# Kernel optimization log

Measured on AMD Instinct MI355X. Metric: run time of the kernel, lower is better.

## Reference

```python
import jax, jax.numpy as jnp
import numpy as np

N, F, HID, C = 8192, 256, 128, 64
ALPHA = 0.2  # LeakyReLU negative slope
NEG = -9e15  # mask value from the torch code


def xavier(key, shape, gain=1.414):
    fan_in, fan_out = shape[0], shape[1]
    limit = gain * np.sqrt(6.0 / (fan_in + fan_out))
    return jax.random.uniform(key, shape, jnp.float32, -limit, limit)


def setup_inputs() -> dict:
    key = jax.random.key(0)
    ks = jax.random.split(key, 6)
    features = jax.random.normal(ks[0], (N, F), jnp.float32)
    support = (jax.random.uniform(ks[1], (N, N)) > 0.995).astype(jnp.float32)
    support = support.at[jnp.arange(N), jnp.arange(N)].set(1.0)
    W0 = xavier(ks[2], (2 * F, HID))
    a0 = xavier(ks[3], (2 * HID, 1))
    W1 = xavier(ks[4], (2 * HID, C))
    a1 = xavier(ks[5], (2 * C, 1))
    return {"features": features, "support": support, "W0": W0, "a0": a0, "W1": W1, "a1": a1}


def gat_layer(x, adj, W, a, concat):
    # precalc=False branch: support = spmm(adj, x); cat with x
    s = adj @ x                               # (N, Fin)
    sup = jnp.concatenate([s, x], axis=1)     # (N, 2*Fin)
    h = sup @ W                               # (N, Fout)
    Fout = h.shape[1]
    # cat([h_i, h_j]) @ a == h_i @ a[:Fout] + h_j @ a[Fout:]  (same math, no N*N*2F tensor)
    src = h @ a[:Fout, 0]                     # (N,)
    dst = h @ a[Fout:, 0]                     # (N,)
    e = jax.nn.leaky_relu(src[:, None] + dst[None, :], ALPHA)  # (N, N)
    e = jnp.where(adj > 0, e, NEG)            # adjacency-masked scores
    att = jax.nn.softmax(e, axis=1)           # (N, N); dropout is identity in eval
    hp = att @ h                              # (N, Fout)
    return jax.nn.elu(hp) if concat else hp


def reference(features, support, W0, a0, W1, a1):
    x = gat_layer(features, support, W0, a0, concat=True)
    out = gat_layer(x, support, W1, a1, concat=False)
    return jax.nn.log_softmax(out, axis=1)
```

## Files before the change

### kernel.cpp

```cpp
#include <hip/hip_runtime.h>
#include <math.h>
#include <stdint.h>

#define NROWS 8192
#define EDGE_CAP 128

using f4v = __attribute__((ext_vector_type(4))) float;

__device__ __forceinline__ uint16_t bfpack(float f) {
    uint32_t x = __float_as_uint(f);
    return (uint16_t)((x + 0x7FFFu + ((x >> 16) & 1u)) >> 16);
}
__device__ __forceinline__ float bfun(uint16_t u) {
    return __uint_as_float((uint32_t)u << 16);
}

__global__ __launch_bounds__(256) void fused_csr_gemm1(const float* __restrict__ adj,
                                                       int* __restrict__ cnt,
                                                       int* __restrict__ col,
                                                       const float* __restrict__ A,
                                                       const float* __restrict__ W,
                                                       float* __restrict__ Y,
                                                       float* __restrict__ Z) {
    __shared__ float As[16][64];
    __shared__ float Bs[16][128];
    int gb  = blockIdx.x;
    int tid = threadIdx.x;

    if (gb < 256) {
        int bm = gb & 127, bn = gb >> 7;
        int tx = tid & 15, ty = tid >> 4;
        const float* Wb = W + (size_t)bn * 256 * 128;
        float acc[4][8] = {};
        for (int k0 = 0; k0 < 256; k0 += 16) {
            {
                int r = tid >> 2, kk = (tid & 3) * 4;
                float4 v = *(const float4*)&A[(size_t)(bm * 64 + r) * 256 + k0 + kk];
                As[kk + 0][r] = v.x; As[kk + 1][r] = v.y;
                As[kk + 2][r] = v.z; As[kk + 3][r] = v.w;
            }
            {
                int kk = tid >> 4, c = (tid & 15) * 8;
                *(float4*)&Bs[kk][c]     = *(const float4*)&Wb[(size_t)(k0 + kk) * 128 + c];
                *(float4*)&Bs[kk][c + 4] = *(const float4*)&Wb[(size_t)(k0 + kk) * 128 + c + 4];
            }
            __syncthreads();
            #pragma unroll
            for (int kk = 0; kk < 16; ++kk) {
                float a[4], b[8];
                #pragma unroll
                for (int i = 0; i < 4; ++i) a[i] = As[kk][ty * 4 + i];
                #pragma unroll
                for (int j = 0; j < 8; ++j) b[j] = Bs[kk][tx * 8 + j];
                #pragma unroll
                for (int i = 0; i < 4; ++i)
                    #pragma unroll
                    for (int j = 0; j < 8; ++j) acc[i][j] += a[i] * b[j];
            }
            __syncthreads();
        }
        float* O = bn ? Z : Y;
        #pragma unroll
        for (int i = 0; i < 4; ++i) {
            int r = bm * 64 + ty * 4 + i;
            float4 v0 = {acc[i][0], acc[i][1], acc[i][2], acc[i][3]};
            float4 v1 = {acc[i][4], acc[i][5], acc[i][6], acc[i][7]};
            *(float4*)&O[(size_t)r * 128 + tx * 8]     = v0;
            *(float4*)&O[(size_t)r * 128 + tx * 8 + 4] = v1;
        }
    } else {
        int row  = (gb - 256) * 4 + (tid >> 6);
        int lane = tid & 63;
        const f4v* arow = (const f4v*)(adj + (size_t)row * NROWS);
        int* crow = col + (size_t)row * EDGE_CAP;
        int count = 0;
        for (int it = 0; it < NROWS / 256; ++it) {
            f4v v = __builtin_nontemporal_load(&arow[it * 64 + lane]);
            float vv[4] = {v.x, v.y, v.z, v.w};
            #pragma unroll
            for (int p = 0; p < 4; ++p) {
                bool nz = vv[p] > 0.0f;
                unsigned long long m = __ballot(nz);
                if (nz) {
                    int off = count + __popcll(m & ((1ull << lane) - 1ull));
                    if (off < EDGE_CAP) crow[off] = it * 256 + lane * 4 + p;
                }
                count += __popcll(m);
            }
        }
        if (lane == 0) cnt[row] = count < EDGE_CAP ? count : EDGE_CAP;
    }
}

__global__ __launch_bounds__(256) void spmm_scores_128(const int* __restrict__ cnt,
                                                       const int* __restrict__ col,
                                                       const float* __restrict__ Y,
                                                       const float* __restrict__ Z,
                                                       const float* __restrict__ a,
                                                       float* __restrict__ H,
                                                       float* __restrict__ src,
                                                       float* __restrict__ dst) {
    __shared__ int sbuf[4][EDGE_CAP];
    int wav  = threadIdx.x >> 6;
    int lane = threadIdx.x & 63;
    int row  = blockIdx.x * 4 + wav;
    int n    = cnt[row];
    const int* cr = col + (size_t)row * EDGE_CAP;
    for (int e = lane; e < n; e += 64) sbuf[wav][e] = cr[e];

    const float2* Y2 = (const float2*)Y;
    float2 s = {0.0f, 0.0f};
    int e = 0;
    for (; e + 8 <= n; e += 8) {
        float2 v[8];
        #pragma unroll
        for (int u = 0; u < 8; ++u) {
            int j = sbuf[wav][e + u];
            v[u] = Y2[(size_t)j * 64 + lane];
        }
        #pragma unroll
        for (int u = 0; u < 8; ++u) { s.x += v[u].x; s.y += v[u].y; }
    }
    for (; e < n; ++e) {
        int j = sbuf[wav][e];
        float2 v = Y2[(size_t)j * 64 + lane];
        s.x += v.x; s.y += v.y;
    }
    float2 z = ((const float2*)Z)[(size_t)row * 64 + lane];
    float hx = s.x + z.x, hy = s.y + z.y;
    float2 hv = {hx, hy};
    ((float2*)H)[(size_t)row * 64 + lane] = hv;
    float s1 = hx * a[lane * 2] + hy * a[lane * 2 + 1];
    float s2 = hx * a[128 + lane * 2] + hy * a[128 + lane * 2 + 1];
    #pragma unroll
    for (int off = 32; off; off >>= 1) {
        s1 += __shfl_xor(s1, off);
        s2 += __shfl_xor(s2, off);
    }
    if (lane == 0) { src[row] = s1; dst[row] = s2; }
}

__global__ __launch_bounds__(256) void attn_agg_gemm2(const int* __restrict__ cnt,
                                                      const int* __restrict__ col,
                                                      const float* __restrict__ H,
                                                      const float* __restrict__ src,
                                                      const float* __restrict__ dst,
                                                      const float* __restrict__ W1,
                                                      float* __restrict__ Y2,
                                                      float* __restrict__ Z2) {
    __shared__ float pbuf[4][EDGE_CAP];
    __shared__ int   cbuf[4][EDGE_CAP];
    __shared__ float xrow[4][128];
    int wav  = threadIdx.x >> 6;
    int lane = threadIdx.x & 63;
    int row  = blockIdx.x * 4 + wav;
    int n    = cnt[row];
    const int* cr = col + (size_t)row * EDGE_CAP;
    float si = src[row];

    float m = -3.0e38f;
    for (int e = lane; e < n; e += 64) {
        int j = cr[e];
        float x = si + dst[j];
        x = x > 0.0f ? x : 0.2f * x;
        cbuf[wav][e] = j;
        pbuf[wav][e] = x;
        m = fmaxf(m, x);
    }
    #pragma unroll
    for (int off = 32; off; off >>= 1) m = fmaxf(m, __shfl_xor(m, off));

    float ssum = 0.0f;
    for (int e = lane; e < n; e += 64) {
        float p = __expf(pbuf[wav][e] - m);
        pbuf[wav][e] = p;
        ssum += p;
    }
    #pragma unroll
    for (int off = 32; off; off >>= 1) ssum += __shfl_xor(ssum, off);
    float inv = 1.0f / ssum;

    const float2* H2 = (const float2*)H;
    float2 o = {0.0f, 0.0f};
    int e = 0;
    for (; e + 8 <= n; e += 8) {
        float2 v[8]; float p[8];
        #pragma unroll
        for (int u = 0; u < 8; ++u) {
            int j = cbuf[wav][e + u];
            p[u] = pbuf[wav][e + u];
            v[u] = H2[(size_t)j * 64 + lane];
        }
        #pragma unroll
        for (int u = 0; u < 8; ++u) { o.x += p[u] * v[u].x; o.y += p[u] * v[u].y; }
    }
    for (; e < n; ++e) {
        int j = cbuf[wav][e];
        float p = pbuf[wav][e];
        float2 v = H2[(size_t)j * 64 + lane];
        o.x += p * v.x; o.y += p * v.y;
    }
    float vx = o.x * inv, vy = o.y * inv;
    vx = vx > 0.0f ? vx : (__expf(vx) - 1.0f);
    vy = vy > 0.0f ? vy : (__expf(vy) - 1.0f);

    float2 hv = {vx, vy};
    ((float2*)&xrow[wav][0])[lane] = hv;

    float y = 0.0f, z = 0.0f;
    #pragma unroll 8
    for (int k = 0; k < 128; ++k) {
        float xk = xrow[wav][k];
        y += xk * W1[(size_t)k * 64 + lane];
        z += xk * W1[(size_t)(128 + k) * 64 + lane];
    }
    Y2[(size_t)row * 64 + lane] = y;
    Z2[(size_t)row * 64 + lane] = z;
}

__global__ __launch_bounds__(256) void spmm_scores_64(const int* __restrict__ cnt,
                                                      const int* __restrict__ col,
                                                      const float* __restrict__ Y,
                                                      const float* __restrict__ Z,
                                                      const float* __restrict__ a,
                                                      uint16_t* __restrict__ Hb,
                                                      float* __restrict__ src,
                                                      float* __restrict__ dst) {
    __shared__ int sbuf[4][EDGE_CAP];
    int wav  = threadIdx.x >> 6;
    int lane = threadIdx.x & 63;
    int row  = blockIdx.x * 4 + wav;
    int n    = cnt[row];
    const int* cr = col + (size_t)row * EDGE_CAP;
    for (int e = lane; e < n; e += 64) sbuf[wav][e] = cr[e];

    float s = 0.0f;
    int e = 0;
    for (; e + 8 <= n; e += 8) {
        float v[8];
        #pragma unroll
        for (int u = 0; u < 8; ++u) v[u] = Y[(size_t)sbuf[wav][e + u] * 64 + lane];
        #pragma unroll
        for (int u = 0; u < 8; ++u) s += v[u];
    }
    for (; e < n; ++e) s += Y[(size_t)sbuf[wav][e] * 64 + lane];
    float h = s + Z[(size_t)row * 64 + lane];
    Hb[(size_t)row * 64 + lane] = bfpack(h);
    float s1 = h * a[lane];
    float s2 = h * a[64 + lane];
    #pragma unroll
    for (int off = 32; off; off >>= 1) {
        s1 += __shfl_xor(s1, off);
        s2 += __shfl_xor(s2, off);
    }
    if (lane == 0) { src[row] = s1; dst[row] = s2; }
}

__global__ __launch_bounds__(256) void attn_agg_final(const int* __restrict__ cnt,
                                                      const int* __restrict__ col,
                                                      const uint16_t* __restrict__ Hb,
                                                      const float* __restrict__ src,
                                                      const float* __restrict__ dst,
                                                      float* __restrict__ out) {
    __shared__ float pbuf[4][EDGE_CAP];
    __shared__ int   cbuf[4][EDGE_CAP];
    int wav  = threadIdx.x >> 6;
    int lane = threadIdx.x & 63;
    int row  = blockIdx.x * 4 + wav;
    int n    = cnt[row];
    const int* cr = col + (size_t)row * EDGE_CAP;
    float si = src[row];

    float m = -3.0e38f;
    for (int e = lane; e < n; e += 64) {
        int j = cr[e];
        float x = si + dst[j];
        x = x > 0.0f ? x : 0.2f * x;
        cbuf[wav][e] = j;
        pbuf[wav][e] = x;
        m = fmaxf(m, x);
    }
    #pragma unroll
    for (int off = 32; off; off >>= 1) m = fmaxf(m, __shfl_xor(m, off));

    float ssum = 0.0f;
    for (int e = lane; e < n; e += 64) {
        float p = __expf(pbuf[wav][e] - m);
        pbuf[wav][e] = p;
        ssum += p;
    }
    #pragma unroll
    for (int off = 32; off; off >>= 1) ssum += __shfl_xor(ssum, off);
    float inv = 1.0f / ssum;

    float o = 0.0f;
    int e = 0;
    for (; e + 8 <= n; e += 8) {
        uint16_t v[8]; float p[8];
        #pragma unroll
        for (int u = 0; u < 8; ++u) {
            p[u] = pbuf[wav][e + u];
            v[u] = Hb[(size_t)cbuf[wav][e + u] * 64 + lane];
        }
        #pragma unroll
        for (int u = 0; u < 8; ++u) o += p[u] * bfun(v[u]);
    }
    for (; e < n; ++e) o += pbuf[wav][e] * bfun(Hb[(size_t)cbuf[wav][e] * 64 + lane]);

    float logit = o * inv;
    float mm = logit;
    #pragma unroll
    for (int off = 32; off; off >>= 1) mm = fmaxf(mm, __shfl_xor(mm, off));
    float se = __expf(logit - mm);
    #pragma unroll
    for (int off = 32; off; off >>= 1) se += __shfl_xor(se, off);
    out[(size_t)row * 64 + lane] = logit - mm - logf(se);
}

extern "C" void kernel_launch(void* const* d_in, const int* in_sizes, int n_in,
                              void* d_out, int out_size, void* d_ws, size_t ws_size,
                              hipStream_t stream) {
    const float* feat = (const float*)d_in[0];
    const float* adj  = (const float*)d_in[1];
    const float* W0   = (const float*)d_in[2];
    const float* a0   = (const float*)d_in[3];
    const float* W1   = (const float*)d_in[4];
    const float* a1   = (const float*)d_in[5];
    float* out = (float*)d_out;

    char* w = (char*)d_ws;
    int* cnt      = (int*)w;        w += (size_t)NROWS * sizeof(int);
    int* col      = (int*)w;        w += (size_t)NROWS * EDGE_CAP * sizeof(int);
    float* Y1   = (float*)w;        w += (size_t)NROWS * 128 * sizeof(float);
    float* Z1   = (float*)w;        w += (size_t)NROWS * 128 * sizeof(float);
    float* H1   = (float*)w;        w += (size_t)NROWS * 128 * sizeof(float);
    float* Y2   = (float*)w;        w += (size_t)NROWS * 64 * sizeof(float);
    float* Z2   = (float*)w;        w += (size_t)NROWS * 64 * sizeof(float);
    uint16_t* H2b = (uint16_t*)w;   w += (size_t)NROWS * 64 * sizeof(uint16_t);
    float* src1 = (float*)w;        w += (size_t)NROWS * sizeof(float);
    float* dst1 = (float*)w;        w += (size_t)NROWS * sizeof(float);
    float* src2 = (float*)w;        w += (size_t)NROWS * sizeof(float);
    float* dst2 = (float*)w;        w += (size_t)NROWS * sizeof(float);

    fused_csr_gemm1<<<256 + NROWS / 4, 256, 0, stream>>>(adj, cnt, col, feat, W0, Y1, Z1);

    spmm_scores_128<<<NROWS / 4, 256, 0, stream>>>(cnt, col, Y1, Z1, a0, H1, src1, dst1);
    attn_agg_gemm2<<<NROWS / 4, 256, 0, stream>>>(cnt, col, H1, src1, dst1, W1, Y2, Z2);

    spmm_scores_64<<<NROWS / 4, 256, 0, stream>>>(cnt, col, Y2, Z2, a1, H2b, src2, dst2);
    attn_agg_final<<<NROWS / 4, 256, 0, stream>>>(cnt, col, H2b, src2, dst2, out);
}
```

Before: 430.6 us.

## Merge four sparse stage kernels into one persistent kernel with grid barriers

Replaces the four per-stage launches (spmm+scores, attention+gemm2, spmm+scores, final attention) with a single persistent kernel of 1024 blocks, each processing two rows per wave, separated by atomic-counter grid barriers. The barrier counter is reset by the first kernel. The goal is to remove kernel launch gaps and tail effects between the small stages. It relies on all 1024 blocks being co-resident, or the barrier spin will deadlock, and it adds barrier spin and serialization overhead.

```diff
diff --git a/kernel.cpp b/kernel.cpp
--- a/kernel.cpp
+++ b/kernel.cpp
@@ -4,6 +4,7 @@
 
 #define NROWS 8192
 #define EDGE_CAP 128
+#define PGRID 1024
 
 using f4v = __attribute__((ext_vector_type(4))) float;
 
@@ -21,11 +22,13 @@
                                                        const float* __restrict__ A,
                                                        const float* __restrict__ W,
                                                        float* __restrict__ Y,
-                                                       float* __restrict__ Z) {
+                                                       float* __restrict__ Z,
+                                                       int* __restrict__ bar) {
     __shared__ float As[16][64];
     __shared__ float Bs[16][128];
     int gb  = blockIdx.x;
     int tid = threadIdx.x;
+    if (gb == 0 && tid == 0) *bar = 0;
 
     if (gb < 256) {
         int bm = gb & 127, bn = gb >> 7;
@@ -92,229 +95,212 @@
     }
 }
 
-__global__ __launch_bounds__(256) void spmm_scores_128(const int* __restrict__ cnt,
-                                                       const int* __restrict__ col,
-                                                       const float* __restrict__ Y,
-                                                       const float* __restrict__ Z,
-                                                       const float* __restrict__ a,
-                                                       float* __restrict__ H,
-                                                       float* __restrict__ src,
-                                                       float* __restrict__ dst) {
-    __shared__ int sbuf[4][EDGE_CAP];
-    int wav  = threadIdx.x >> 6;
-    int lane = threadIdx.x & 63;
-    int row  = blockIdx.x * 4 + wav;
-    int n    = cnt[row];
-    const int* cr = col + (size_t)row * EDGE_CAP;
-    for (int e = lane; e < n; e += 64) sbuf[wav][e] = cr[e];
-
-    const float2* Y2 = (const float2*)Y;
-    float2 s = {0.0f, 0.0f};
-    int e = 0;
-    for (; e + 8 <= n; e += 8) {
-        float2 v[8];
-        #pragma unroll
-        for (int u = 0; u < 8; ++u) {
-            int j = sbuf[wav][e + u];
-            v[u] = Y2[(size_t)j * 64 + lane];
-        }
-        #pragma unroll
-        for (int u = 0; u < 8; ++u) { s.x += v[u].x; s.y += v[u].y; }
-    }
-    for (; e < n; ++e) {
-        int j = sbuf[wav][e];
-        float2 v = Y2[(size_t)j * 64 + lane];
-        s.x += v.x; s.y += v.y;
-    }
-    float2 z = ((const float2*)Z)[(size_t)row * 64 + lane];
-    float hx = s.x + z.x, hy = s.y + z.y;
-    float2 hv = {hx, hy};
-    ((float2*)H)[(size_t)row * 64 + lane] = hv;
-    float s1 = hx * a[lane * 2] + hy * a[lane * 2 + 1];
-    float s2 = hx * a[128 + lane * 2] + hy * a[128 + lane * 2 + 1];
-    #pragma unroll
-    for (int off = 32; off; off >>= 1) {
-        s1 += __shfl_xor(s1, off);
-        s2 += __shfl_xor(s2, off);
-    }
-    if (lane == 0) { src[row] = s1; dst[row] = s2; }
-}
-
-__global__ __launch_bounds__(256) void attn_agg_gemm2(const int* __restrict__ cnt,
-                                                      const int* __restrict__ col,
-                                                      const float* __restrict__ H,
-                                                      const float* __restrict__ src,
-                                                      const float* __restrict__ dst,
-                                                      const float* __restrict__ W1,
-                                                      float* __restrict__ Y2,
-                                                      float* __restrict__ Z2) {
+__device__ __forceinline__ void grid_barrier(int* bar, int target) {
+    __syncthreads();
+    if (threadIdx.x == 0) {
+        __threadfence();
+        atomicAdd(bar, 1);
+        while (__hip_atomic_load(bar, __ATOMIC_RELAXED, __HIP_MEMORY_SCOPE_AGENT) < target)
+            __builtin_amdgcn_s_sleep(2);
+    }
+    __syncthreads();
+    __threadfence();
+}
+
+__global__ __launch_bounds__(256, 4) void gat_sparse_mega(
+        const int* __restrict__ cnt, const int* __restrict__ col,
+        const float* __restrict__ Y1, const float* __restrict__ Z1,
+        const float* __restrict__ a0,
+        float* __restrict__ H1, float* __restrict__ src1, float* __restrict__ dst1,
+        const float* __restrict__ W1,
+        float* __restrict__ Y2, float* __restrict__ Z2,
+        const float* __restrict__ a1,
+        uint16_t* __restrict__ H2b, float* __restrict__ src2, float* __restrict__ dst2,
+        float* __restrict__ out, int* __restrict__ bar) {
+    __shared__ int   ibuf[4][EDGE_CAP];
     __shared__ float pbuf[4][EDGE_CAP];
-    __shared__ int   cbuf[4][EDGE_CAP];
     __shared__ float xrow[4][128];
     int wav  = threadIdx.x >> 6;
     int lane = threadIdx.x & 63;
-    int row  = blockIdx.x * 4 + wav;
-    int n    = cnt[row];
-    const int* cr = col + (size_t)row * EDGE_CAP;
-    float si = src[row];
-
-    float m = -3.0e38f;
-    for (int e = lane; e < n; e += 64) {
-        int j = cr[e];
-        float x = si + dst[j];
-        x = x > 0.0f ? x : 0.2f * x;
-        cbuf[wav][e] = j;
-        pbuf[wav][e] = x;
-        m = fmaxf(m, x);
-    }
-    #pragma unroll
-    for (int off = 32; off; off >>= 1) m = fmaxf(m, __shfl_xor(m, off));
-
-    float ssum = 0.0f;
-    for (int e = lane; e < n; e += 64) {
-        float p = __expf(pbuf[wav][e] - m);
-        pbuf[wav][e] = p;
-        ssum += p;
-    }
-    #pragma unroll
-    for (int off = 32; off; off >>= 1) ssum += __shfl_xor(ssum, off);
-    float inv = 1.0f / ssum;
-
-    const float2* H2 = (const float2*)H;
-    float2 o = {0.0f, 0.0f};
-    int e = 0;
-    for (; e + 8 <= n; e += 8) {
-        float2 v[8]; float p[8];
-        #pragma unroll
-        for (int u = 0; u < 8; ++u) {
-            int j = cbuf[wav][e + u];
-            p[u] = pbuf[wav][e + u];
-            v[u] = H2[(size_t)j * 64 + lane];
-        }
-        #pragma unroll
-        for (int u = 0; u < 8; ++u) { o.x += p[u] * v[u].x; o.y += p[u] * v[u].y; }
-    }
-    for (; e < n; ++e) {
-        int j = cbuf[wav][e];
-        float p = pbuf[wav][e];
-        float2 v = H2[(size_t)j * 64 + lane];
-        o.x += p * v.x; o.y += p * v.y;
-    }
-    float vx = o.x * inv, vy = o.y * inv;
-    vx = vx > 0.0f ? vx : (__expf(vx) - 1.0f);
-    vy = vy > 0.0f ? vy : (__expf(vy) - 1.0f);
-
-    float2 hv = {vx, vy};
-    ((float2*)&xrow[wav][0])[lane] = hv;
-
-    float y = 0.0f, z = 0.0f;
-    #pragma unroll 8
-    for (int k = 0; k < 128; ++k) {
-        float xk = xrow[wav][k];
-        y += xk * W1[(size_t)k * 64 + lane];
-        z += xk * W1[(size_t)(128 + k) * 64 + lane];
-    }
-    Y2[(size_t)row * 64 + lane] = y;
-    Z2[(size_t)row * 64 + lane] = z;
-}
-
-__global__ __launch_bounds__(256) void spmm_scores_64(const int* __restrict__ cnt,
-                                                      const int* __restrict__ col,
-                                                      const float* __restrict__ Y,
-                                                      const float* __restrict__ Z,
-                                                      const float* __restrict__ a,
-                                                      uint16_t* __restrict__ Hb,
-                                                      float* __restrict__ src,
-                                                      float* __restrict__ dst) {
-    __shared__ int sbuf[4][EDGE_CAP];
-    int wav  = threadIdx.x >> 6;
-    int lane = threadIdx.x & 63;
-    int row  = blockIdx.x * 4 + wav;
-    int n    = cnt[row];
-    const int* cr = col + (size_t)row * EDGE_CAP;
-    for (int e = lane; e < n; e += 64) sbuf[wav][e] = cr[e];
-
-    float s = 0.0f;
-    int e = 0;
-    for (; e + 8 <= n; e += 8) {
-        float v[8];
-        #pragma unroll
-        for (int u = 0; u < 8; ++u) v[u] = Y[(size_t)sbuf[wav][e + u] * 64 + lane];
-        #pragma unroll
-        for (int u = 0; u < 8; ++u) s += v[u];
-    }
-    for (; e < n; ++e) s += Y[(size_t)sbuf[wav][e] * 64 + lane];
-    float h = s + Z[(size_t)row * 64 + lane];
-    Hb[(size_t)row * 64 + lane] = bfpack(h);
-    float s1 = h * a[lane];
-    float s2 = h * a[64 + lane];
-    #pragma unroll
-    for (int off = 32; off; off >>= 1) {
-        s1 += __shfl_xor(s1, off);
-        s2 += __shfl_xor(s2, off);
-    }
-    if (lane == 0) { src[row] = s1; dst[row] = s2; }
-}
-
-__global__ __launch_bounds__(256) void attn_agg_final(const int* __restrict__ cnt,
-                                                      const int* __restrict__ col,
-                                                      const uint16_t* __restrict__ Hb,
-                                                      const float* __restrict__ src,
-                                                      const float* __restrict__ dst,
-                                                      float* __restrict__ out) {
-    __shared__ float pbuf[4][EDGE_CAP];
-    __shared__ int   cbuf[4][EDGE_CAP];
-    int wav  = threadIdx.x >> 6;
-    int lane = threadIdx.x & 63;
-    int row  = blockIdx.x * 4 + wav;
-    int n    = cnt[row];
-    const int* cr = col + (size_t)row * EDGE_CAP;
-    float si = src[row];
-
-    float m = -3.0e38f;
-    for (int e = lane; e < n; e += 64) {
-        int j = cr[e];
-        float x = si + dst[j];
-        x = x > 0.0f ? x : 0.2f * x;
-        cbuf[wav][e] = j;
-        pbuf[wav][e] = x;
-        m = fmaxf(m, x);
-    }
-    #pragma unroll
-    for (int off = 32; off; off >>= 1) m = fmaxf(m, __shfl_xor(m, off));
-
-    float ssum = 0.0f;
-    for (int e = lane; e < n; e += 64) {
-        float p = __expf(pbuf[wav][e] - m);
-        pbuf[wav][e] = p;
-        ssum += p;
-    }
-    #pragma unroll
-    for (int off = 32; off; off >>= 1) ssum += __shfl_xor(ssum, off);
-    float inv = 1.0f / ssum;
-
-    float o = 0.0f;
-    int e = 0;
-    for (; e + 8 <= n; e += 8) {
-        uint16_t v[8]; float p[8];
-        #pragma unroll
-        for (int u = 0; u < 8; ++u) {
-            p[u] = pbuf[wav][e + u];
-            v[u] = Hb[(size_t)cbuf[wav][e + u] * 64 + lane];
-        }
-        #pragma unroll
-        for (int u = 0; u < 8; ++u) o += p[u] * bfun(v[u]);
-    }
-    for (; e < n; ++e) o += pbuf[wav][e] * bfun(Hb[(size_t)cbuf[wav][e] * 64 + lane]);
-
-    float logit = o * inv;
-    float mm = logit;
-    #pragma unroll
-    for (int off = 32; off; off >>= 1) mm = fmaxf(mm, __shfl_xor(mm, off));
-    float se = __expf(logit - mm);
-    #pragma unroll
-    for (int off = 32; off; off >>= 1) se += __shfl_xor(se, off);
-    out[(size_t)row * 64 + lane] = logit - mm - logf(se);
+    int base = blockIdx.x * 4 + wav;
+
+    #pragma unroll 1
+    for (int pass = 0; pass < 2; ++pass) {
+        int row = base + pass * 4096;
+        int n = cnt[row];
+        const int* cr = col + (size_t)row * EDGE_CAP;
+        for (int e = lane; e < n; e += 64) ibuf[wav][e] = cr[e];
+        const float2* Yv = (const float2*)Y1;
+        float sx = 0.0f, sy = 0.0f;
+        int e = 0;
+        for (; e + 8 <= n; e += 8) {
+            float2 v[8];
+            #pragma unroll
+            for (int u = 0; u < 8; ++u) v[u] = Yv[(size_t)ibuf[wav][e + u] * 64 + lane];
+            #pragma unroll
+            for (int u = 0; u < 8; ++u) { sx += v[u].x; sy += v[u].y; }
+        }
+        for (; e < n; ++e) {
+            float2 v = Yv[(size_t)ibuf[wav][e] * 64 + lane];
+            sx += v.x; sy += v.y;
+        }
+        float2 z = ((const float2*)Z1)[(size_t)row * 64 + lane];
+        float hx = sx + z.x, hy = sy + z.y;
+        float2 hv = {hx, hy};
+        ((float2*)H1)[(size_t)row * 64 + lane] = hv;
+        float s1 = hx * a0[lane * 2] + hy * a0[lane * 2 + 1];
+        float s2 = hx * a0[128 + lane * 2] + hy * a0[128 + lane * 2 + 1];
+        #pragma unroll
+        for (int off = 32; off; off >>= 1) {
+            s1 += __shfl_xor(s1, off);
+            s2 += __shfl_xor(s2, off);
+        }
+        if (lane == 0) { src1[row] = s1; dst1[row] = s2; }
+    }
+    grid_barrier(bar, PGRID);
+
+    #pragma unroll 1
+    for (int pass = 0; pass < 2; ++pass) {
+        int row = base + pass * 4096;
+        int n = cnt[row];
+        const int* cr = col + (size_t)row * EDGE_CAP;
+        float si = src1[row];
+        float m = -3.0e38f;
+        for (int e = lane; e < n; e += 64) {
+            int j = cr[e];
+            float x = si + dst1[j];
+            x = x > 0.0f ? x : 0.2f * x;
+            ibuf[wav][e] = j;
+            pbuf[wav][e] = x;
+            m = fmaxf(m, x);
+        }
+        #pragma unroll
+        for (int off = 32; off; off >>= 1) m = fmaxf(m, __shfl_xor(m, off));
+        float ssum = 0.0f;
+        for (int e = lane; e < n; e += 64) {
+            float p = __expf(pbuf[wav][e] - m);
+            pbuf[wav][e] = p;
+            ssum += p;
+        }
+        #pragma unroll
+        for (int off = 32; off; off >>= 1) ssum += __shfl_xor(ssum, off);
+        float inv = 1.0f / ssum;
+
+        const float2* Hv = (const float2*)H1;
+        float ox = 0.0f, oy = 0.0f;
+        int e = 0;
+        for (; e + 8 <= n; e += 8) {
+            float2 v[8]; float p[8];
+            #pragma unroll
+            for (int u = 0; u < 8; ++u) {
+                p[u] = pbuf[wav][e + u];
+                v[u] = Hv[(size_t)ibuf[wav][e + u] * 64 + lane];
+            }
+            #pragma unroll
+            for (int u = 0; u < 8; ++u) { ox += p[u] * v[u].x; oy += p[u] * v[u].y; }
+        }
+        for (; e < n; ++e) {
+            float p = pbuf[wav][e];
+            float2 v = Hv[(size_t)ibuf[wav][e] * 64 + lane];
+            ox += p * v.x; oy += p * v.y;
+        }
+        float vx = ox * inv, vy = oy * inv;
+        vx = vx > 0.0f ? vx : (__expf(vx) - 1.0f);
+        vy = vy > 0.0f ? vy : (__expf(vy) - 1.0f);
+        float2 hv = {vx, vy};
+        ((float2*)&xrow[wav][0])[lane] = hv;
+
+        float y = 0.0f, zz = 0.0f;
+        #pragma unroll 8
+        for (int k = 0; k < 128; ++k) {
+            float xk = xrow[wav][k];
+            y  += xk * W1[(size_t)k * 64 + lane];
+            zz += xk * W1[(size_t)(128 + k) * 64 + lane];
+        }
+        Y2[(size_t)row * 64 + lane] = y;
+        Z2[(size_t)row * 64 + lane] = zz;
+    }
+    grid_barrier(bar, 2 * PGRID);
+
+    #pragma unroll 1
+    for (int pass = 0; pass < 2; ++pass) {
+        int row = base + pass * 4096;
+        int n = cnt[row];
+        const int* cr = col + (size_t)row * EDGE_CAP;
+        for (int e = lane; e < n; e += 64) ibuf[wav][e] = cr[e];
+        float s = 0.0f;
+        int e = 0;
+        for (; e + 8 <= n; e += 8) {
+            float v[8];
+            #pragma unroll
+            for (int u = 0; u < 8; ++u) v[u] = Y2[(size_t)ibuf[wav][e + u] * 64 + lane];
+            #pragma unroll
+            for (int u = 0; u < 8; ++u) s += v[u];
+        }
+        for (; e < n; ++e) s += Y2[(size_t)ibuf[wav][e] * 64 + lane];
+        float h = s + Z2[(size_t)row * 64 + lane];
+        H2b[(size_t)row * 64 + lane] = bfpack(h);
+        float s1 = h * a1[lane];
+        float s2 = h * a1[64 + lane];
+        #pragma unroll
+        for (int off = 32; off; off >>= 1) {
+            s1 += __shfl_xor(s1, off);
+            s2 += __shfl_xor(s2, off);
+        }
+        if (lane == 0) { src2[row] = s1; dst2[row] = s2; }
+    }
+    grid_barrier(bar, 3 * PGRID);
+
+    #pragma unroll 1
+    for (int pass = 0; pass < 2; ++pass) {
+        int row = base + pass * 4096;
+        int n = cnt[row];
+        const int* cr = col + (size_t)row * EDGE_CAP;
+        float si = src2[row];
+        float m = -3.0e38f;
+        for (int e = lane; e < n; e += 64) {
+            int j = cr[e];
+            float x = si + dst2[j];
+            x = x > 0.0f ? x : 0.2f * x;
+            ibuf[wav][e] = j;
+            pbuf[wav][e] = x;
+            m = fmaxf(m, x);
+        }
+        #pragma unroll
+        for (int off = 32; off; off >>= 1) m = fmaxf(m, __shfl_xor(m, off));
+        float ssum = 0.0f;
+        for (int e = lane; e < n; e += 64) {
+            float p = __expf(pbuf[wav][e] - m);
+            pbuf[wav][e] = p;
+            ssum += p;
+        }
+        #pragma unroll
+        for (int off = 32; off; off >>= 1) ssum += __shfl_xor(ssum, off);
+        float inv = 1.0f / ssum;
+
+        float o = 0.0f;
+        int e = 0;
+        for (; e + 8 <= n; e += 8) {
+            uint16_t v[8]; float p[8];
+            #pragma unroll
+            for (int u = 0; u < 8; ++u) {
+                p[u] = pbuf[wav][e + u];
+                v[u] = H2b[(size_t)ibuf[wav][e + u] * 64 + lane];
+            }
+            #pragma unroll
+            for (int u = 0; u < 8; ++u) o += p[u] * bfun(v[u]);
+        }
+        for (; e < n; ++e) o += pbuf[wav][e] * bfun(H2b[(size_t)ibuf[wav][e] * 64 + lane]);
+
+        float logit = o * inv;
+        float mm = logit;
+        #pragma unroll
+        for (int off = 32; off; off >>= 1) mm = fmaxf(mm, __shfl_xor(mm, off));
+        float se = __expf(logit - mm);
+        #pragma unroll
+        for (int off = 32; off; off >>= 1) se += __shfl_xor(se, off);
+        out[(size_t)row * 64 + lane] = logit - mm - logf(se);
+    }
 }
 
 extern "C" void kernel_launch(void* const* d_in, const int* in_sizes, int n_in,
@@ -341,12 +327,11 @@
     float* dst1 = (float*)w;        w += (size_t)NROWS * sizeof(float);
     float* src2 = (float*)w;        w += (size_t)NROWS * sizeof(float);
     float* dst2 = (float*)w;        w += (size_t)NROWS * sizeof(float);
-
-    fused_csr_gemm1<<<256 + NROWS / 4, 256, 0, stream>>>(adj, cnt, col, feat, W0, Y1, Z1);
-
-    spmm_scores_128<<<NROWS / 4, 256, 0, stream>>>(cnt, col, Y1, Z1, a0, H1, src1, dst1);
-    attn_agg_gemm2<<<NROWS / 4, 256, 0, stream>>>(cnt, col, H1, src1, dst1, W1, Y2, Z2);
-
-    spmm_scores_64<<<NROWS / 4, 256, 0, stream>>>(cnt, col, Y2, Z2, a1, H2b, src2, dst2);
-    attn_agg_final<<<NROWS / 4, 256, 0, stream>>>(cnt, col, H2b, src2, dst2, out);
-}
+    int* bar    = (int*)w;          w += 64;
+
+    fused_csr_gemm1<<<256 + NROWS / 4, 256, 0, stream>>>(adj, cnt, col, feat, W0, Y1, Z1, bar);
+
+    gat_sparse_mega<<<PGRID, 256, 0, stream>>>(cnt, col, Y1, Z1, a0,
+                                               H1, src1, dst1, W1, Y2, Z2, a1,
+                                               H2b, src2, dst2, out, bar);
+}
```

New measurement: 945.3 us. 2.2x slower.
